# Kernel optimization log

Hardware: AMD Instinct MI355X
Metric: run time of the kernel (lower is better)

## Reference

```python
import jax, jax.numpy as jnp
import numpy as np

INPUT_EMB, KQ_EMB, V_EMB = 1024, 64, 64

def setup_inputs() -> dict:
    key = jax.random.key(0)
    k1, k2, k3, k4 = jax.random.split(key, 4)
    x = jax.random.normal(k1, (4, 2048, INPUT_EMB), dtype=jnp.float32)
    # nn.Linear weights: [out, in], applied as x @ W.T
    Wq = jax.random.normal(k2, (KQ_EMB, INPUT_EMB), dtype=jnp.float32) * (INPUT_EMB ** -0.5)
    Wk = jax.random.normal(k3, (KQ_EMB, INPUT_EMB), dtype=jnp.float32) * (INPUT_EMB ** -0.5)
    Wv = jax.random.normal(k4, (V_EMB, INPUT_EMB), dtype=jnp.float32) * (INPUT_EMB ** -0.5)
    return {"x": x, "Wq": Wq, "Wk": Wk, "Wv": Wv}

def reference(x, Wq, Wk, Wv):
    # Q,K: [b, s, kq], V: [b, s, v]
    Q = jnp.einsum('bsd,ed->bse', x, Wq)
    K = jnp.einsum('bsd,ed->bse', x, Wk)
    V = jnp.einsum('bsd,ed->bse', x, Wv)
    scale = 1.0 / (KQ_EMB ** 0.5)
    scores = jnp.einsum('bqe,bke->bqk', Q, K) * scale  # [b, s, s]
    attn = jax.nn.softmax(scores, axis=-1)
    return jnp.einsum('bqk,bkv->bqv', attn, V)
```

## Files before the change

kernel.cpp:

```cpp
#include <hip/hip_runtime.h>
#include <hip/hip_bf16.h>

typedef __bf16 bf16x8 __attribute__((ext_vector_type(8)));
typedef __bf16 bf16x4 __attribute__((ext_vector_type(4)));
typedef float floatx4 __attribute__((ext_vector_type(4)));

#define LOG2E 1.44269504088896340736f
#define NS 8

__global__ void wconv_kernel(const float* __restrict__ Wq,
                             const float* __restrict__ Wk,
                             const float* __restrict__ Wv,
                             __bf16* __restrict__ Wc) {
    int row = blockIdx.x;
    int c0  = threadIdx.x * 4;
    const float* src; float scale;
    if (row < 64)       { src = Wq + (size_t)row * 1024;         scale = 0.125f * LOG2E; }
    else if (row < 128) { src = Wk + (size_t)(row - 64) * 1024;  scale = 1.0f; }
    else                { src = Wv + (size_t)(row - 128) * 1024; scale = 1.0f; }
    float4 v = *(const float4*)(src + c0);
    bf16x4 o;
    o[0] = (__bf16)(v.x * scale);
    o[1] = (__bf16)(v.y * scale);
    o[2] = (__bf16)(v.z * scale);
    o[3] = (__bf16)(v.w * scale);
    *(bf16x4*)(Wc + (size_t)row * 1024 + c0) = o;
}

__global__ __launch_bounds__(512) void qkv_kernel(const float* __restrict__ x,
                                                  const __bf16* __restrict__ Wc,
                                                  __bf16* __restrict__ Qb,
                                                  __bf16* __restrict__ Kb,
                                                  __bf16* __restrict__ Vt) {
    __shared__ __align__(16) __bf16 Alds[32 * 1040];
    const int tid = threadIdx.x;
    const int w = tid >> 6, lane = tid & 63;
    const int quad = lane >> 4, l15 = lane & 15;
    const int nw = w & 3, kw = w >> 2;
    const int rowbase = blockIdx.x * 32;

    const float* xb = x + (size_t)rowbase * 1024;
#pragma unroll
    for (int it = 0; it < 16; ++it) {
        int i = tid + 512 * it;
        int r = i >> 8, c = (i & 255) * 4;
        float4 v = *(const float4*)(xb + r * 1024 + c);
        bf16x4 o;
        o[0] = (__bf16)v.x; o[1] = (__bf16)v.y; o[2] = (__bf16)v.z; o[3] = (__bf16)v.w;
        *(bf16x4*)&Alds[r * 1040 + c] = o;
    }
    __syncthreads();

    floatx4 acc[2][3];
#pragma unroll
    for (int f = 0; f < 2; ++f)
#pragma unroll
        for (int nt = 0; nt < 3; ++nt) acc[f][nt] = (floatx4)0.0f;

    const int kk0 = kw * 16;
    const __bf16* Bp[3];
#pragma unroll
    for (int nt = 0; nt < 3; ++nt) {
        int c = nw * 48 + nt * 16 + l15;
        Bp[nt] = Wc + (size_t)c * 1024 + quad * 8;
    }
    bf16x8 Bc[3];
#pragma unroll
    for (int nt = 0; nt < 3; ++nt) Bc[nt] = *(const bf16x8*)(Bp[nt] + kk0 * 32);

#pragma unroll
    for (int t = 0; t < 16; ++t) {
        const int kk = kk0 + t;
        bf16x8 Bn[3];
        if (t < 15) {
#pragma unroll
            for (int nt = 0; nt < 3; ++nt) Bn[nt] = *(const bf16x8*)(Bp[nt] + (kk + 1) * 32);
        }
        bf16x8 a0 = *(const bf16x8*)&Alds[l15 * 1040 + kk * 32 + quad * 8];
        bf16x8 a1 = *(const bf16x8*)&Alds[(16 + l15) * 1040 + kk * 32 + quad * 8];
#pragma unroll
        for (int nt = 0; nt < 3; ++nt) {
            acc[0][nt] = __builtin_amdgcn_mfma_f32_16x16x32_bf16(a0, Bc[nt], acc[0][nt], 0, 0, 0);
            acc[1][nt] = __builtin_amdgcn_mfma_f32_16x16x32_bf16(a1, Bc[nt], acc[1][nt], 0, 0, 0);
        }
#pragma unroll
        for (int nt = 0; nt < 3; ++nt) Bc[nt] = Bn[nt];
    }

    __syncthreads();
    float* red = (float*)Alds;
    if (kw == 1) {
#pragma unroll
        for (int f = 0; f < 2; ++f)
#pragma unroll
            for (int nt = 0; nt < 3; ++nt)
#pragma unroll
                for (int r = 0; r < 4; ++r) {
                    int row = f * 16 + quad * 4 + r, col = nt * 16 + l15;
                    red[nw * 1664 + row * 52 + col] = acc[f][nt][r];
                }
    }
    __syncthreads();
    if (kw == 0) {
#pragma unroll
        for (int f = 0; f < 2; ++f)
#pragma unroll
            for (int nt = 0; nt < 3; ++nt) {
                int c = nw * 48 + nt * 16 + l15;
#pragma unroll
                for (int r = 0; r < 4; ++r) {
                    int row = f * 16 + quad * 4 + r;
                    float vsum = acc[f][nt][r] + red[nw * 1664 + row * 52 + nt * 16 + l15];
                    int grow = rowbase + row;
                    int b = grow >> 11, s = grow & 2047;
                    __bf16 val = (__bf16)vsum;
                    if (c < 64)       Qb[((size_t)b * 2048 + s) * 64 + c] = val;
                    else if (c < 128) Kb[((size_t)b * 2048 + s) * 64 + (c - 64)] = val;
                    else              Vt[((size_t)b * 64 + (c - 128)) * 2048 + s] = val;
                }
            }
    }
}

__global__ __launch_bounds__(256) void attn_kernel(const __bf16* __restrict__ Qb,
                                                   const __bf16* __restrict__ Kb,
                                                   const __bf16* __restrict__ Vt,
                                                   float* __restrict__ Opart,
                                                   float* __restrict__ lpart) {
    __shared__ __align__(16) char smem[4 * 16 * 64 * 4 + 4 * 16 * 4];
    __bf16 (*plds)[16][72] = (__bf16 (*)[16][72])smem;
    float (*lO)[16][64]    = (float (*)[16][64])smem;
    float* ll              = (float*)(smem + 16384);

    const int tid = threadIdx.x;
    const int w = tid >> 6, lane = tid & 63;
    const int quad = lane >> 4, l15 = lane & 15;
    const int qsub = w & 1, kw = w >> 1;
    const int qt = blockIdx.x >> 3;
    const int ks = blockIdx.x & (NS - 1);
    const int bb = qt >> 6, qloc = qt & 63;
    const int grow0 = bb * 2048 + qloc * 32 + qsub * 16;

    const __bf16* Qp = Qb + (size_t)(grow0 + l15) * 64 + quad * 8;
    bf16x8 aq0 = *(const bf16x8*)(Qp);
    bf16x8 aq1 = *(const bf16x8*)(Qp + 32);

    float l[4] = {0.f, 0.f, 0.f, 0.f};
    floatx4 O[4];
#pragma unroll
    for (int vt = 0; vt < 4; ++vt) O[vt] = (floatx4)0.0f;

    const __bf16* Kbase = Kb + (size_t)bb * 2048 * 64;
    const __bf16* Vbase = Vt + (size_t)bb * 64 * 2048;
    const int kcb0 = (ks * 2 + kw) * 128;

#pragma unroll
    for (int t = 0; t < 2; ++t) {
        const int kcb = kcb0 + t * 64;
        floatx4 s[4];
#pragma unroll
        for (int nt = 0; nt < 4; ++nt) s[nt] = (floatx4)0.0f;
#pragma unroll
        for (int nt = 0; nt < 4; ++nt) {
            const __bf16* kp = Kbase + (size_t)(kcb + nt * 16 + l15) * 64 + quad * 8;
            bf16x8 b0 = *(const bf16x8*)(kp);
            bf16x8 b1 = *(const bf16x8*)(kp + 32);
            s[nt] = __builtin_amdgcn_mfma_f32_16x16x32_bf16(aq0, b0, s[nt], 0, 0, 0);
            s[nt] = __builtin_amdgcn_mfma_f32_16x16x32_bf16(aq1, b1, s[nt], 0, 0, 0);
        }
#pragma unroll
        for (int nt = 0; nt < 4; ++nt) {
#pragma unroll
            for (int r = 0; r < 4; ++r) {
                float p = exp2f(s[nt][r]);
                l[r] += p;
                plds[w][quad * 4 + r][nt * 16 + l15] = (__bf16)p;
            }
        }
        bf16x8 pa0 = *(const bf16x8*)&plds[w][l15][quad * 8];
        bf16x8 pa1 = *(const bf16x8*)&plds[w][l15][32 + quad * 8];
#pragma unroll
        for (int vt = 0; vt < 4; ++vt) {
            const __bf16* vp = Vbase + (size_t)(vt * 16 + l15) * 2048 + kcb + quad * 8;
            bf16x8 b0 = *(const bf16x8*)(vp);
            bf16x8 b1 = *(const bf16x8*)(vp + 32);
            O[vt] = __builtin_amdgcn_mfma_f32_16x16x32_bf16(pa0, b0, O[vt], 0, 0, 0);
            O[vt] = __builtin_amdgcn_mfma_f32_16x16x32_bf16(pa1, b1, O[vt], 0, 0, 0);
        }
    }

#pragma unroll
    for (int r = 0; r < 4; ++r) {
        l[r] += __shfl_xor(l[r], 1);
        l[r] += __shfl_xor(l[r], 2);
        l[r] += __shfl_xor(l[r], 4);
        l[r] += __shfl_xor(l[r], 8);
    }

    __syncthreads();
#pragma unroll
    for (int r = 0; r < 4; ++r) {
        int row = quad * 4 + r;
        if (l15 == 0) ll[w * 16 + row] = l[r];
#pragma unroll
        for (int vt = 0; vt < 4; ++vt) lO[w][row][vt * 16 + l15] = O[vt][r];
    }
    __syncthreads();
    if (kw == 0) {
#pragma unroll
        for (int r = 0; r < 4; ++r) {
            int row = quad * 4 + r;
            float lsum = l[r] + ll[(w + 2) * 16 + row];
            if (l15 == 0) lpart[(size_t)ks * 8192 + grow0 + row] = lsum;
#pragma unroll
            for (int vt = 0; vt < 4; ++vt) {
                float o = O[vt][r] + lO[w + 2][row][vt * 16 + l15];
                Opart[((size_t)ks * 8192 + grow0 + row) * 64 + vt * 16 + l15] = o;
            }
        }
    }
}

__global__ __launch_bounds__(256) void combine_kernel(const float* __restrict__ Opart,
                                                      const float* __restrict__ lpart,
                                                      float* __restrict__ out) {
    int idx4 = blockIdx.x * 256 + threadIdx.x;
    int row = idx4 >> 4;
    float4 o = make_float4(0.f, 0.f, 0.f, 0.f);
    float l = 0.f;
#pragma unroll
    for (int ks = 0; ks < NS; ++ks) {
        float4 p = *(const float4*)(Opart + (size_t)ks * 524288 + (size_t)idx4 * 4);
        o.x += p.x; o.y += p.y; o.z += p.z; o.w += p.w;
        l += lpart[(size_t)ks * 8192 + row];
    }
    float inv = 1.0f / l;
    float4 r = make_float4(o.x * inv, o.y * inv, o.z * inv, o.w * inv);
    *(float4*)(out + (size_t)idx4 * 4) = r;
}

extern "C" void kernel_launch(void* const* d_in, const int* in_sizes, int n_in,
                              void* d_out, int out_size, void* d_ws, size_t ws_size,
                              hipStream_t stream) {
    const float* x  = (const float*)d_in[0];
    const float* Wq = (const float*)d_in[1];
    const float* Wk = (const float*)d_in[2];
    const float* Wv = (const float*)d_in[3];
    float* out = (float*)d_out;

    char* ws = (char*)d_ws;
    __bf16* Wc = (__bf16*)ws;
    __bf16* Qb = (__bf16*)(ws + 393216);
    __bf16* Kb = (__bf16*)(ws + 393216 + 2097152);
    __bf16* Vt = (__bf16*)(ws + 393216 + 2 * 2097152);
    size_t base = 393216 + 3 * 2097152;
    float* Opart = (float*)(ws + base);
    float* lpart = (float*)(ws + base + (size_t)NS * 524288 * 4);

    wconv_kernel<<<192, 256, 0, stream>>>(Wq, Wk, Wv, Wc);
    qkv_kernel<<<256, 512, 0, stream>>>(x, Wc, Qb, Kb, Vt);
    attn_kernel<<<256 * NS, 256, 0, stream>>>(Qb, Kb, Vt, Opart, lpart);
    combine_kernel<<<512, 256, 0, stream>>>(Opart, lpart, out);
}
```

Before: 131.7 us.

## Store Q/K/V in MFMA fragment-native layout via LDS-staged coalesced writes

The QKV projection now stages its bf16 outputs in shared memory and writes them to global memory as contiguous 16-byte-per-lane fragments, pre-arranged in the operand layout the attention kernel's MFMA loads expect. The attention kernel then reads Q, K and V fragments with fully contiguous lane*8 loads instead of strided row/column gathers. The old path did scattered scalar bf16 stores, with V transposed at a 2048-element stride. The change adds an extra LDS round trip and barrier in the projection kernel and couples both kernels to a fixed fragment layout. The workspace shrinks because the tensors were previously over-allocated.

```diff
diff --git a/kernel.cpp b/kernel.cpp
--- a/kernel.cpp
+++ b/kernel.cpp
@@ -7,6 +7,7 @@
 
 #define LOG2E 1.44269504088896340736f
 #define NS 8
+
 
 __global__ void wconv_kernel(const float* __restrict__ Wq,
                              const float* __restrict__ Wk,
@@ -29,9 +30,9 @@
 
 __global__ __launch_bounds__(512) void qkv_kernel(const float* __restrict__ x,
                                                   const __bf16* __restrict__ Wc,
-                                                  __bf16* __restrict__ Qb,
-                                                  __bf16* __restrict__ Kb,
-                                                  __bf16* __restrict__ Vt) {
+                                                  __bf16* __restrict__ Qf,
+                                                  __bf16* __restrict__ Kf,
+                                                  __bf16* __restrict__ Vf) {
     __shared__ __align__(16) __bf16 Alds[32 * 1040];
     const int tid = threadIdx.x;
     const int w = tid >> 6, lane = tid & 63;
@@ -88,7 +89,10 @@
     }
 
     __syncthreads();
-    float* red = (float*)Alds;
+    float*  red    = (float*)Alds;
+    __bf16* TileQK = (__bf16*)((char*)Alds + 26624);
+    __bf16* TileV  = (__bf16*)((char*)Alds + 35328);
+
     if (kw == 1) {
 #pragma unroll
         for (int f = 0; f < 2; ++f)
@@ -111,20 +115,35 @@
                 for (int r = 0; r < 4; ++r) {
                     int row = f * 16 + quad * 4 + r;
                     float vsum = acc[f][nt][r] + red[nw * 1664 + row * 52 + nt * 16 + l15];
-                    int grow = rowbase + row;
-                    int b = grow >> 11, s = grow & 2047;
                     __bf16 val = (__bf16)vsum;
-                    if (c < 64)       Qb[((size_t)b * 2048 + s) * 64 + c] = val;
-                    else if (c < 128) Kb[((size_t)b * 2048 + s) * 64 + (c - 64)] = val;
-                    else              Vt[((size_t)b * 64 + (c - 128)) * 2048 + s] = val;
+                    if (c < 128) TileQK[row * 136 + c] = val;
+                    else         TileV[(c - 128) * 40 + row] = val;
                 }
             }
     }
-}
-
-__global__ __launch_bounds__(256) void attn_kernel(const __bf16* __restrict__ Qb,
-                                                   const __bf16* __restrict__ Kb,
-                                                   const __bf16* __restrict__ Vt,
+    __syncthreads();
+    for (int st = w; st < 12; st += 8) {
+        bf16x8 frag;
+        __bf16* gdst;
+        if (st < 8) {
+            int tile = (st & 3) >> 1, h = st & 1;
+            int colbase = (st < 4 ? 0 : 64) + h * 32 + quad * 8;
+            frag = *(const bf16x8*)&TileQK[(tile * 16 + l15) * 136 + colbase];
+            size_t g16 = (size_t)blockIdx.x * 2 + tile;
+            __bf16* basep = (st < 4) ? Qf : Kf;
+            gdst = basep + (g16 * 2 + h) * 512 + lane * 8;
+        } else {
+            int vt = st - 8;
+            frag = *(const bf16x8*)&TileV[(vt * 16 + l15) * 40 + quad * 8];
+            gdst = Vf + ((size_t)blockIdx.x * 4 + vt) * 512 + lane * 8;
+        }
+        *(bf16x8*)gdst = frag;
+    }
+}
+
+__global__ __launch_bounds__(256) void attn_kernel(const __bf16* __restrict__ Qf,
+                                                   const __bf16* __restrict__ Kf,
+                                                   const __bf16* __restrict__ Vf,
                                                    float* __restrict__ Opart,
                                                    float* __restrict__ lpart) {
     __shared__ __align__(16) char smem[4 * 16 * 64 * 4 + 4 * 16 * 4];
@@ -141,30 +160,30 @@
     const int bb = qt >> 6, qloc = qt & 63;
     const int grow0 = bb * 2048 + qloc * 32 + qsub * 16;
 
-    const __bf16* Qp = Qb + (size_t)(grow0 + l15) * 64 + quad * 8;
+    const __bf16* Qp = Qf + (size_t)(grow0 >> 4) * 1024 + lane * 8;
     bf16x8 aq0 = *(const bf16x8*)(Qp);
-    bf16x8 aq1 = *(const bf16x8*)(Qp + 32);
+    bf16x8 aq1 = *(const bf16x8*)(Qp + 512);
 
     float l[4] = {0.f, 0.f, 0.f, 0.f};
     floatx4 O[4];
 #pragma unroll
     for (int vt = 0; vt < 4; ++vt) O[vt] = (floatx4)0.0f;
 
-    const __bf16* Kbase = Kb + (size_t)bb * 2048 * 64;
-    const __bf16* Vbase = Vt + (size_t)bb * 64 * 2048;
     const int kcb0 = (ks * 2 + kw) * 128;
 
 #pragma unroll
     for (int t = 0; t < 2; ++t) {
         const int kcb = kcb0 + t * 64;
+        const int k16 = bb * 128 + (kcb >> 4);
+        const int k32 = bb * 64 + (kcb >> 5);
         floatx4 s[4];
 #pragma unroll
         for (int nt = 0; nt < 4; ++nt) s[nt] = (floatx4)0.0f;
 #pragma unroll
         for (int nt = 0; nt < 4; ++nt) {
-            const __bf16* kp = Kbase + (size_t)(kcb + nt * 16 + l15) * 64 + quad * 8;
+            const __bf16* kp = Kf + (size_t)(k16 + nt) * 1024 + lane * 8;
             bf16x8 b0 = *(const bf16x8*)(kp);
-            bf16x8 b1 = *(const bf16x8*)(kp + 32);
+            bf16x8 b1 = *(const bf16x8*)(kp + 512);
             s[nt] = __builtin_amdgcn_mfma_f32_16x16x32_bf16(aq0, b0, s[nt], 0, 0, 0);
             s[nt] = __builtin_amdgcn_mfma_f32_16x16x32_bf16(aq1, b1, s[nt], 0, 0, 0);
         }
@@ -181,9 +200,9 @@
         bf16x8 pa1 = *(const bf16x8*)&plds[w][l15][32 + quad * 8];
 #pragma unroll
         for (int vt = 0; vt < 4; ++vt) {
-            const __bf16* vp = Vbase + (size_t)(vt * 16 + l15) * 2048 + kcb + quad * 8;
+            const __bf16* vp = Vf + (size_t)(k32 * 4 + vt) * 512 + lane * 8;
             bf16x8 b0 = *(const bf16x8*)(vp);
-            bf16x8 b1 = *(const bf16x8*)(vp + 32);
+            bf16x8 b1 = *(const bf16x8*)(vp + 2048);
             O[vt] = __builtin_amdgcn_mfma_f32_16x16x32_bf16(pa0, b0, O[vt], 0, 0, 0);
             O[vt] = __builtin_amdgcn_mfma_f32_16x16x32_bf16(pa1, b1, O[vt], 0, 0, 0);
         }
@@ -250,15 +269,15 @@
 
     char* ws = (char*)d_ws;
     __bf16* Wc = (__bf16*)ws;
-    __bf16* Qb = (__bf16*)(ws + 393216);
-    __bf16* Kb = (__bf16*)(ws + 393216 + 2097152);
-    __bf16* Vt = (__bf16*)(ws + 393216 + 2 * 2097152);
-    size_t base = 393216 + 3 * 2097152;
+    __bf16* Qf = (__bf16*)(ws + 393216);
+    __bf16* Kf = (__bf16*)(ws + 393216 + 1048576);
+    __bf16* Vf = (__bf16*)(ws + 393216 + 2 * 1048576);
+    size_t base = 393216 + 3 * 1048576;
     float* Opart = (float*)(ws + base);
     float* lpart = (float*)(ws + base + (size_t)NS * 524288 * 4);
 
     wconv_kernel<<<192, 256, 0, stream>>>(Wq, Wk, Wv, Wc);
-    qkv_kernel<<<256, 512, 0, stream>>>(x, Wc, Qb, Kb, Vt);
-    attn_kernel<<<256 * NS, 256, 0, stream>>>(Qb, Kb, Vt, Opart, lpart);
+    qkv_kernel<<<256, 512, 0, stream>>>(x, Wc, Qf, Kf, Vf);
+    attn_kernel<<<256 * NS, 256, 0, stream>>>(Qf, Kf, Vf, Opart, lpart);
     combine_kernel<<<512, 256, 0, stream>>>(Opart, lpart, out);
 }
```

Result: faster. 110.8 us (median of 2 runs) (-15.8%).
